# Kernel tuning notes

Measured on AMD Instinct MI355X. Metric: run time of the kernel, lower is better.

## Reference

```python
import jax, jax.numpy as jnp
from jax import lax
import numpy as np

# 6D tensors: (N, C, h1, w1, h2, w2); weights: (Cout, Cin, k,k,k,k)
DN = lax.ConvDimensionNumbers(lhs_spec=(0, 1, 2, 3, 4, 5),
                              rhs_spec=(0, 1, 2, 3, 4, 5),
                              out_spec=(0, 1, 2, 3, 4, 5))


def conv4d_relu(x, w, b):
    # true 4D convolution, stride 1, SAME padding, then bias + ReLU
    y = lax.conv_general_dilated(x, w, window_strides=(1, 1, 1, 1),
                                 padding='SAME', dimension_numbers=DN)
    return jax.nn.relu(y + b.reshape(1, -1, 1, 1, 1, 1))


def _perm(x):
    # swap the two (h, w) spatial pairs of the correlation tensor
    return jnp.transpose(x, (0, 1, 4, 5, 2, 3))


def _sym(x, w, b):
    # symmetric_mode branch: f(x) + perm(f(perm(x)))
    return conv4d_relu(x, w, b) + _perm(conv4d_relu(_perm(x), w, b))


def setup_inputs() -> dict:
    key = jax.random.key(0)
    ks = jax.random.split(key, 9)
    B, S = 4, 20
    sc = 0.05
    return {
        'x':    jax.random.normal(ks[0], (B, 1, S, S, S, S), dtype=jnp.float32),
        'w0':   jax.random.normal(ks[1], (16, 1, 5, 5, 5, 5), dtype=jnp.float32) * sc,
        'b0':   jax.random.normal(ks[2], (16,), dtype=jnp.float32) * sc,
        'w10':  jax.random.normal(ks[3], (8, 16, 3, 3, 5, 5), dtype=jnp.float32) * sc,
        'b10':  jax.random.normal(ks[4], (8,), dtype=jnp.float32) * sc,
        'w11':  jax.random.normal(ks[5], (8, 16, 5, 5, 5, 5), dtype=jnp.float32) * sc,
        'b11':  jax.random.normal(ks[6], (8,), dtype=jnp.float32) * sc,
        'w2':   jax.random.normal(ks[7], (1, 16, 5, 5, 5, 5), dtype=jnp.float32) * sc,
        'b2':   jax.random.normal(ks[8], (1,), dtype=jnp.float32) * sc,
    }


def reference(x, w0, b0, w10, b10, w11, b11, w2, b2):
    x = _sym(x, w0, b0)                       # [B,16,S,S,S,S]
    x0 = _sym(x, w10, b10)                    # [B, 8,S,S,S,S]
    x1 = _sym(x, w11, b11)                    # [B, 8,S,S,S,S]
    x = jnp.concatenate((x0, x1), axis=1)     # [B,16,S,S,S,S]
    return _sym(x, w2, b2)                    # [B, 1,S,S,S,S]
```

## Files before the change

### kernel.cpp

```cpp
#include <hip/hip_runtime.h>

#define TS 20
#define TS2 400

typedef __attribute__((ext_vector_type(8))) __bf16 bf16x8;
typedef __attribute__((ext_vector_type(4))) __bf16 bf16x4;
typedef __attribute__((ext_vector_type(4))) float  f32x4;
typedef __attribute__((ext_vector_type(4))) int    int4v;

__device__ __forceinline__ float relu_f(float v) { return v > 0.0f ? v : 0.0f; }

#define MFMA16(a, b, c) __builtin_amdgcn_mfma_f32_16x16x32_bf16((a), (b), (c), 0, 0, 0)

#define LPAD 580

__global__ __launch_bounds__(256)
void pack_w0(const float* __restrict__ w0, __bf16* __restrict__ wpk0)
{
    int idx = blockIdx.x * 256 + (int)threadIdx.x;
    if (idx >= 25 * 32 * 32) return;
    const int c = idx & 31;
    const int m = (idx >> 5) & 31;
    const int e = idx >> 10;
    float v = 0.0f;
    if (c < 25) {
        const int co = m & 15;
        const int k1o = c / 5, k2o = c % 5, k3i = e / 5, k4i = e % 5;
        if (m < 16) v = w0[co * 625 + k1o * 125 + k2o * 25 + k3i * 5 + k4i];
        else        v = w0[co * 625 + k3i * 125 + k4i * 25 + k1o * 5 + k2o];
    }
    wpk0[idx] = (__bf16)v;
}

__global__ __launch_bounds__(256)
void pack_wmid(const float* __restrict__ w10, const float* __restrict__ w11,
               __bf16* __restrict__ wpk)
{
    int idx = blockIdx.x * 256 + (int)threadIdx.x;
    if (idx >= 650 * 512) return;
    const int ci  = idx & 15;
    const int m   = (idx >> 4) & 31;
    const int off = idx >> 9;
    const int inner = off % 26, outer = off / 26;
    const int d1 = outer / 5 - 2, d2 = outer % 5 - 2;
    float v = 0.0f;
    if (inner < 25) {
        const int d3 = inner / 5 - 2, d4 = inner % 5 - 2;
        const int co = m & 7;
        const bool isB  = (m & 8)  != 0;
        const bool is11 = (m & 16) != 0;
        if (is11) {
            int k1, k2, k3, k4;
            if (!isB) { k1 = d1 + 2; k2 = d2 + 2; k3 = d3 + 2; k4 = d4 + 2; }
            else      { k1 = d3 + 2; k2 = d4 + 2; k3 = d1 + 2; k4 = d2 + 2; }
            v = w11[((((co * 16 + ci) * 5 + k1) * 5 + k2) * 5 + k3) * 5 + k4];
        } else {
            if (!isB) {
                if (d1 >= -1 && d1 <= 1 && d2 >= -1 && d2 <= 1)
                    v = w10[((((co * 16 + ci) * 3 + (d1 + 1)) * 3 + (d2 + 1)) * 5 + (d3 + 2)) * 5 + (d4 + 2)];
            } else {
                if (d3 >= -1 && d3 <= 1 && d4 >= -1 && d4 <= 1)
                    v = w10[((((co * 16 + ci) * 3 + (d3 + 1)) * 3 + (d4 + 1)) * 5 + (d1 + 2)) * 5 + (d2 + 2)];
            }
        }
    }
    wpk[idx] = (__bf16)v;
}

__global__ __launch_bounds__(256)
void pack_w2f(const float* __restrict__ w2, __bf16* __restrict__ wpk2f)
{
    int idx = blockIdx.x * 256 + (int)threadIdx.x;
    if (idx >= 26 * 64 * 16) return;
    const int ci = idx & 15;
    const int m  = (idx >> 4) & 63;
    const int e  = idx >> 10;
    float v = 0.0f;
    if (e < 25) {
        if (m < 25)
            v = w2[ci * 625 + (m / 5) * 125 + (m % 5) * 25 + (e / 5) * 5 + (e % 5)];
        else if (m >= 32 && m < 57) {
            const int dd = m - 32;
            v = w2[ci * 625 + (e / 5) * 125 + (e % 5) * 25 + (dd / 5) * 5 + (dd % 5)];
        }
    }
    wpk2f[idx] = (__bf16)v;
}

__global__ __launch_bounds__(320)
void conv0_mfma(const float* __restrict__ x, const __bf16* __restrict__ wpk0,
                const float* __restrict__ b0, __bf16* __restrict__ y1)
{
    __shared__ __bf16 lds0[4 * LPAD * 8];

    const int tid  = (int)threadIdx.x;
    const int lane = tid & 63;
    const int wave = tid >> 6;
    const int bid  = blockIdx.x;
    const int o2 = bid % TS, o1 = (bid / TS) % TS, n = bid / TS2;

    for (int i = tid; i < 4 * LPAD * 8 / 2; i += 320) ((int*)lds0)[i] = 0;
    __syncthreads();

    for (int c = tid; c < 25 * TS2; c += 320) {
        const int pl = c / TS2, pt = c % TS2;
        const int i1 = o1 + pl / 5 - 2, i2 = o2 + pl % 5 - 2;
        if (i1 >= 0 && i1 < TS && i2 >= 0 && i2 < TS) {
            const float v = x[(size_t)((n * TS + i1) * TS + i2) * TS2 + pt];
            const int L = (pt / TS + 2) * 24 + (pt % TS + 2);
            lds0[((pl >> 3) * LPAD + L) * 8 + (pl & 7)] = (__bf16)v;
        }
    }
    __syncthreads();

    const int mrow = lane & 15;
    const int sub  = lane >> 4;

    int sb[5];
#pragma unroll
    for (int i = 0; i < 5; ++i) {
        const int p = (wave * 5 + i) * 16 + mrow;
        sb[i] = (sub * LPAD + (p / TS + 2) * 24 + (p % TS + 2)) * 8;
    }

    f32x4 acc0[5], acc1[5];
#pragma unroll
    for (int i = 0; i < 5; ++i) {
        acc0[i] = (f32x4){0.f, 0.f, 0.f, 0.f};
        acc1[i] = (f32x4){0.f, 0.f, 0.f, 0.f};
    }

    bf16x8 a0 = *(const bf16x8*)(wpk0 + (size_t)mrow * 32 + sub * 8);
    bf16x8 a1 = *(const bf16x8*)(wpk0 + (size_t)(16 + mrow) * 32 + sub * 8);
    for (int e = 0; e < 25; ++e) {
        bf16x8 na0 = a0, na1 = a1;
        if (e < 24) {
            na0 = *(const bf16x8*)(wpk0 + ((size_t)((e + 1) * 32 + mrow)) * 32 + sub * 8);
            na1 = *(const bf16x8*)(wpk0 + ((size_t)((e + 1) * 32 + 16 + mrow)) * 32 + sub * 8);
        }
        const int delta = ((e / 5 - 2) * 24 + (e % 5 - 2)) * 8;
#pragma unroll
        for (int i = 0; i < 5; ++i) {
            bf16x8 bfr = *(const bf16x8*)(&lds0[sb[i] + delta]);
            acc0[i] = MFMA16(a0, bfr, acc0[i]);
            acc1[i] = MFMA16(a1, bfr, acc1[i]);
        }
        a0 = na0; a1 = na1;
    }

    const f32x4 bv = *(const f32x4*)(b0 + sub * 4);
#pragma unroll
    for (int i = 0; i < 5; ++i) {
        const int p = (wave * 5 + i) * 16 + mrow;
        bf16x4 pk;
#pragma unroll
        for (int r = 0; r < 4; ++r)
            pk[r] = (__bf16)(relu_f(acc0[i][r] + bv[r]) + relu_f(acc1[i][r] + bv[r]));
        *(bf16x4*)(y1 + ((size_t)bid * TS2 + p) * 16 + sub * 4) = pk;
    }
}

__global__ __launch_bounds__(320)
void conv4d_mid_mfma(const __bf16* __restrict__ y1, const __bf16* __restrict__ wpk,
                     const float* __restrict__ b10, const float* __restrict__ b11,
                     __bf16* __restrict__ y2)
{
    __shared__ __bf16 lds[4][9216];

    const int tid  = (int)threadIdx.x;
    const int lane = tid & 63;
    const int wave = tid >> 6;
    const int bid0 = blockIdx.x;
    const int bid  = (bid0 & 7) * 200 + (bid0 >> 3);
    const int o2 = bid % TS, o1 = (bid / TS) % TS, n = bid / TS2;

    for (int i = tid; i < 4 * 9216 / 2; i += 320) ((int*)lds)[i] = 0;

    const int mrow = lane & 15;
    const int sub  = lane >> 4;
    const int ci0  = (sub & 1) * 8;
    const int aoff = (sub >> 1) * 512 + mrow * 16 + ci0;

    int sbase[5];
#pragma unroll
    for (int i = 0; i < 5; ++i) {
        const int p  = (wave * 5 + i) * 16 + mrow;
        sbase[i] = ((p / TS + 2) * 24 + (p % TS + 2)) * 16 + ci0;
    }

    f32x4 acc[5][2];
#pragma unroll
    for (int i = 0; i < 5; ++i) {
        acc[i][0] = (f32x4){0.f, 0.f, 0.f, 0.f};
        acc[i][1] = (f32x4){0.f, 0.f, 0.f, 0.f};
    }

    const __bf16* ybase = y1 + (size_t)n * TS2 * TS2 * 16;

    auto nextv = [&](int k) {
        while (k < 25) {
            const int i1 = o1 + k / 5 - 2, i2 = o2 + k % 5 - 2;
            if (i1 >= 0 && i1 < TS && i2 >= 0 && i2 < TS) break;
            ++k;
        }
        return k;
    };
    auto stage = [&](int k, int bi) {
        const __bf16* src = ybase + (size_t)((o1 + k / 5 - 2) * TS + (o2 + k % 5 - 2)) * TS2 * 16;
        for (int c = tid; c < 800; c += 320) {
            const int h = c / 40, rem = c % 40;
            *(int4v*)(&lds[bi][((h + 2) * 24 + 2) * 16 + rem * 8]) =
                *(const int4v*)(src + c * 8);
        }
    };
    auto compute = [&](int k, int bi) {
        const __bf16* wbase = wpk + (size_t)k * 26 * 512;
        bf16x8 a0 = *(const bf16x8*)(wbase + aoff);
        bf16x8 a1 = *(const bf16x8*)(wbase + aoff + 256);
        for (int ic = 0; ic < 13; ++ic) {
            bf16x8 na0 = a0, na1 = a1;
            if (ic < 12) {
                na0 = *(const bf16x8*)(wbase + (ic + 1) * 1024 + aoff);
                na1 = *(const bf16x8*)(wbase + (ic + 1) * 1024 + aoff + 256);
            }
            const int e = 2 * ic + (sub >> 1);
            int d3 = 0, d4 = 0;
            if (e < 25) { d3 = e / 5 - 2; d4 = e % 5 - 2; }
            const int delta = (d3 * 24 + d4) * 16;
#pragma unroll
            for (int i = 0; i < 5; ++i) {
                bf16x8 bfr = *(const bf16x8*)(&lds[bi][sbase[i] + delta]);
                acc[i][0] = MFMA16(a0, bfr, acc[i][0]);
                acc[i][1] = MFMA16(a1, bfr, acc[i][1]);
            }
            a0 = na0; a1 = na1;
        }
    };

    __syncthreads();

    int kk = nextv(0);
    int pair = 0;
    while (kk < 25) {
        const int k2 = nextv(kk + 1);
        stage(kk, 2 * pair);
        if (k2 < 25) stage(k2, 2 * pair + 1);
        __syncthreads();
        compute(kk, 2 * pair);
        if (k2 < 25) compute(k2, 2 * pair + 1);
        pair ^= 1;
        kk = (k2 < 25) ? nextv(k2 + 1) : 25;
    }

    const size_t base = (size_t)bid * TS2 * 16;
#pragma unroll
    for (int i = 0; i < 5; ++i) {
        const int p = (wave * 5 + i) * 16 + mrow;
#pragma unroll
        for (int mt = 0; mt < 2; ++mt) {
            const float* bs = mt ? b11 : b10;
            const f32x4 bv = *(const f32x4*)(bs + (sub & 1) * 4);
            bf16x4 pk;
#pragma unroll
            for (int r = 0; r < 4; ++r) {
                float v = relu_f(acc[i][mt][r] + bv[r]);
                float o = v + __shfl_xor(v, 32);
                pk[r] = (__bf16)o;
            }
            if (lane < 32)
                *(bf16x4*)(y2 + base + (size_t)p * 16 + mt * 8 + (sub & 1) * 4) = pk;
        }
    }
}

__global__ __launch_bounds__(320)
void conv2t_mfma(const __bf16* __restrict__ y2, const __bf16* __restrict__ wpk2f,
                 int n0, __bf16* __restrict__ t)
{
    __shared__ __bf16 lds[2 * LPAD * 8];

    const int tid  = (int)threadIdx.x;
    const int lane = tid & 63;
    const int wave = tid >> 6;
    const int bid = blockIdx.x;
    const int q2 = bid % TS, q1 = (bid / TS) % TS, nl = bid / TS2;

    for (int i = tid; i < 2 * LPAD * 8 / 2; i += 320) ((int*)lds)[i] = 0;
    __syncthreads();

    const __bf16* src = y2 + (size_t)(((n0 + nl) * TS + q1) * TS + q2) * TS2 * 16;
    for (int c = tid; c < 800; c += 320) {
        const int h = c / 40, rem = c % 40;
        const int w = rem >> 1, cb = rem & 1;
        int4v v = *(const int4v*)(src + c * 8);
        *(int4v*)(&lds[(cb * LPAD + (h + 2) * 24 + 2 + w) * 8]) = v;
    }
    __syncthreads();

    const int mrow = lane & 15;
    const int sub  = lane >> 4;

    int sbase[5];
#pragma unroll
    for (int i = 0; i < 5; ++i) {
        const int p  = (wave * 5 + i) * 16 + mrow;
        sbase[i] = ((sub & 1) * LPAD + (p / TS + 2) * 24 + (p % TS + 2)) * 8;
    }

    f32x4 acc[5][4];
#pragma unroll
    for (int i = 0; i < 5; ++i)
#pragma unroll
        for (int mt = 0; mt < 4; ++mt)
            acc[i][mt] = (f32x4){0.f, 0.f, 0.f, 0.f};

    for (int ic = 0; ic < 13; ++ic) {
        const int e = 2 * ic + (sub >> 1);
        int d3 = 0, d4 = 0;
        if (e < 25) { d3 = e / 5 - 2; d4 = e % 5 - 2; }
        const int delta = (d3 * 24 + d4) * 8;
        const __bf16* abase = wpk2f + ((size_t)e * 64 + mrow) * 16 + (sub & 1) * 8;
        bf16x8 a0 = *(const bf16x8*)(abase);
        bf16x8 a1 = *(const bf16x8*)(abase + 256);
        bf16x8 a2 = *(const bf16x8*)(abase + 512);
        bf16x8 a3 = *(const bf16x8*)(abase + 768);
#pragma unroll
        for (int i = 0; i < 5; ++i) {
            bf16x8 bfr = *(const bf16x8*)(&lds[sbase[i] + delta]);
            acc[i][0] = MFMA16(a0, bfr, acc[i][0]);
            acc[i][1] = MFMA16(a1, bfr, acc[i][1]);
            acc[i][2] = MFMA16(a2, bfr, acc[i][2]);
            acc[i][3] = MFMA16(a3, bfr, acc[i][3]);
        }
    }

    __bf16* tb = t + (size_t)((nl * TS + q1) * TS + q2) * (50 * TS2);
#pragma unroll
    for (int i = 0; i < 5; ++i) {
        const int p = (wave * 5 + i) * 16 + mrow;
#pragma unroll
        for (int mt = 0; mt < 4; ++mt) {
#pragma unroll
            for (int r = 0; r < 4; ++r) {
                const int gm = mt * 16 + sub * 4 + r;
                int m50 = -1;
                if (gm < 25) m50 = gm;
                else if (gm >= 32 && gm < 57) m50 = gm - 7;
                if (m50 >= 0) tb[m50 * TS2 + p] = (__bf16)acc[i][mt][r];
            }
        }
    }
}

__global__ __launch_bounds__(448)
void conv2_sum(const __bf16* __restrict__ t, const float* __restrict__ b2,
               int n0, float* __restrict__ out)
{
    const int tid = (int)threadIdx.x;
    if (tid >= TS2) return;
    const int bid = blockIdx.x;
    const int o2 = bid % TS, o1 = (bid / TS) % TS, nl = bid / TS2;

    float accA = 0.0f, accB = 0.0f;
    for (int dd = 0; dd < 25; ++dd) {
        const int q1 = o1 + dd / 5 - 2, q2 = o2 + dd % 5 - 2;
        if (q1 < 0 || q1 >= TS || q2 < 0 || q2 >= TS) continue;
        const __bf16* tb = t + (size_t)((nl * TS + q1) * TS + q2) * (50 * TS2) + tid;
        accA += (float)tb[dd * TS2];
        accB += (float)tb[(25 + dd) * TS2];
    }
    const float bias = b2[0];
    out[(size_t)(n0 + nl) * (TS2 * (size_t)TS2) + (size_t)(o1 * TS + o2) * TS2 + tid] =
        relu_f(accA + bias) + relu_f(accB + bias);
}

extern "C" void kernel_launch(void* const* d_in, const int* in_sizes, int n_in,
                              void* d_out, int out_size, void* d_ws, size_t ws_size,
                              hipStream_t stream)
{
    const float* x   = (const float*)d_in[0];
    const float* w0  = (const float*)d_in[1];
    const float* b0  = (const float*)d_in[2];
    const float* w10 = (const float*)d_in[3];
    const float* b10 = (const float*)d_in[4];
    const float* w11 = (const float*)d_in[5];
    const float* b11 = (const float*)d_in[6];
    const float* w2  = (const float*)d_in[7];
    const float* b2  = (const float*)d_in[8];
    float* out = (float*)d_out;

    __bf16* y1    = (__bf16*)d_ws;
    __bf16* y2    = y1 + (size_t)10240000;
    __bf16* tbuf  = y2 + (size_t)10240000;
    __bf16* wpkm  = tbuf + (size_t)16000000;
    __bf16* wpk0  = wpkm + 650 * 512;
    __bf16* wpk2f = wpk0 + 25 * 32 * 32;

    dim3 blk320(320), blk256(256), blk448(448);

    pack_w0  <<<dim3((25600 + 255) / 256),  blk256, 0, stream>>>(w0, wpk0);
    pack_wmid<<<dim3((332800 + 255) / 256), blk256, 0, stream>>>(w10, w11, wpkm);
    pack_w2f <<<dim3((26624 + 255) / 256),  blk256, 0, stream>>>(w2, wpk2f);

    conv0_mfma     <<<dim3(4 * TS * TS), blk320, 0, stream>>>(x, wpk0, b0, y1);
    conv4d_mid_mfma<<<dim3(1600),        blk320, 0, stream>>>(y1, wpkm, b10, b11, y2);

    for (int n0 = 0; n0 < 4; n0 += 2) {
        conv2t_mfma<<<dim3(800), blk320, 0, stream>>>(y2, wpk2f, n0, tbuf);
        conv2_sum  <<<dim3(800), blk448, 0, stream>>>(tbuf, b2, n0, out);
    }
}
```

Measured before the change: 604.3 us.

## Store y1 zero-padded and stream per-wave slices to LDS with async loads

conv0 now writes y1 into zero-padded 24x24 planes, cleared beforehand by a new zero kernel, so the mid conv needs no halo handling or LDS clearing. Each wave of the mid conv fetches only the rows its pixels need into its own double-buffered LDS region, using global_load_lds direct-to-LDS transfers. This removes the block-wide __syncthreads and the register staging, and lets each wave prefetch the next input plane while computing the current one. The cost is an extra zero-fill pass over a larger padded buffer, overlapping halo rows loaded by several waves, and a dependence on correct wait handling for the async LDS loads.

Measured after the change: 658.7 us. +9.0%, slower.

```diff
diff --git a/kernel.cpp b/kernel.cpp
--- a/kernel.cpp
+++ b/kernel.cpp
@@ -2,6 +2,7 @@
 
 #define TS 20
 #define TS2 400
+#define PLANE 9216
 
 typedef __attribute__((ext_vector_type(8))) __bf16 bf16x8;
 typedef __attribute__((ext_vector_type(4))) __bf16 bf16x4;
@@ -11,6 +12,13 @@
 __device__ __forceinline__ float relu_f(float v) { return v > 0.0f ? v : 0.0f; }
 
 #define MFMA16(a, b, c) __builtin_amdgcn_mfma_f32_16x16x32_bf16((a), (b), (c), 0, 0, 0)
+
+__device__ __forceinline__ void gload_lds16(const __bf16* g, __bf16* l)
+{
+    __builtin_amdgcn_global_load_lds(
+        (const __attribute__((address_space(1))) void*)g,
+        (__attribute__((address_space(3))) void*)l, 16, 0, 0);
+}
 
 #define LPAD 580
 
@@ -87,6 +95,14 @@
     wpk2f[idx] = (__bf16)v;
 }
 
+__global__ __launch_bounds__(256)
+void zero_y1p(int4v* __restrict__ dst, int n16)
+{
+    const int stride = gridDim.x * 256;
+    for (int i = blockIdx.x * 256 + (int)threadIdx.x; i < n16; i += stride)
+        dst[i] = (int4v){0, 0, 0, 0};
+}
+
 __global__ __launch_bounds__(320)
 void conv0_mfma(const float* __restrict__ x, const __bf16* __restrict__ wpk0,
                 const float* __restrict__ b0, __bf16* __restrict__ y1)
@@ -152,11 +168,12 @@
 #pragma unroll
     for (int i = 0; i < 5; ++i) {
         const int p = (wave * 5 + i) * 16 + mrow;
+        const int Lp = (p / TS + 2) * 24 + (p % TS + 2);
         bf16x4 pk;
 #pragma unroll
         for (int r = 0; r < 4; ++r)
             pk[r] = (__bf16)(relu_f(acc0[i][r] + bv[r]) + relu_f(acc1[i][r] + bv[r]));
-        *(bf16x4*)(y1 + ((size_t)bid * TS2 + p) * 16 + sub * 4) = pk;
+        *(bf16x4*)(y1 + (size_t)bid * PLANE + Lp * 16 + sub * 4) = pk;
     }
 }
 
@@ -165,7 +182,7 @@
                      const float* __restrict__ b10, const float* __restrict__ b11,
                      __bf16* __restrict__ y2)
 {
-    __shared__ __bf16 lds[4][9216];
+    __shared__ __bf16 lds[5][2][3072];
 
     const int tid  = (int)threadIdx.x;
     const int lane = tid & 63;
@@ -174,8 +191,6 @@
     const int bid  = (bid0 & 7) * 200 + (bid0 >> 3);
     const int o2 = bid % TS, o1 = (bid / TS) % TS, n = bid / TS2;
 
-    for (int i = tid; i < 4 * 9216 / 2; i += 320) ((int*)lds)[i] = 0;
-
     const int mrow = lane & 15;
     const int sub  = lane >> 4;
     const int ci0  = (sub & 1) * 8;
@@ -184,8 +199,8 @@
     int sbase[5];
 #pragma unroll
     for (int i = 0; i < 5; ++i) {
-        const int p  = (wave * 5 + i) * 16 + mrow;
-        sbase[i] = ((p / TS + 2) * 24 + (p % TS + 2)) * 16 + ci0;
+        const int pl = i * 16 + mrow;
+        sbase[i] = ((pl / TS + 2) * 24 + (pl % TS + 2)) * 16 + ci0;
     }
 
     f32x4 acc[5][2];
@@ -195,7 +210,8 @@
         acc[i][1] = (f32x4){0.f, 0.f, 0.f, 0.f};
     }
 
-    const __bf16* ybase = y1 + (size_t)n * TS2 * TS2 * 16;
+    const __bf16* ybase = y1 + (size_t)n * TS2 * PLANE;
+    const int sliceoff = wave * 1536 + lane * 8;
 
     auto nextv = [&](int k) {
         while (k < 25) {
@@ -205,15 +221,14 @@
         }
         return k;
     };
-    auto stage = [&](int k, int bi) {
-        const __bf16* src = ybase + (size_t)((o1 + k / 5 - 2) * TS + (o2 + k % 5 - 2)) * TS2 * 16;
-        for (int c = tid; c < 800; c += 320) {
-            const int h = c / 40, rem = c % 40;
-            *(int4v*)(&lds[bi][((h + 2) * 24 + 2) * 16 + rem * 8]) =
-                *(const int4v*)(src + c * 8);
-        }
+    auto dma = [&](int k, int b) {
+        const __bf16* src = ybase
+            + (size_t)((o1 + k / 5 - 2) * TS + (o2 + k % 5 - 2)) * PLANE + sliceoff;
+#pragma unroll
+        for (int i = 0; i < 6; ++i)
+            gload_lds16(src + i * 512, &lds[wave][b][i * 512]);
     };
-    auto compute = [&](int k, int bi) {
+    auto compute = [&](int k, int b) {
         const __bf16* wbase = wpk + (size_t)k * 26 * 512;
         bf16x8 a0 = *(const bf16x8*)(wbase + aoff);
         bf16x8 a1 = *(const bf16x8*)(wbase + aoff + 256);
@@ -229,7 +244,7 @@
             const int delta = (d3 * 24 + d4) * 16;
 #pragma unroll
             for (int i = 0; i < 5; ++i) {
-                bf16x8 bfr = *(const bf16x8*)(&lds[bi][sbase[i] + delta]);
+                bf16x8 bfr = *(const bf16x8*)(&lds[wave][b][sbase[i] + delta]);
                 acc[i][0] = MFMA16(a0, bfr, acc[i][0]);
                 acc[i][1] = MFMA16(a1, bfr, acc[i][1]);
             }
@@ -237,19 +252,17 @@
         }
     };
 
-    __syncthreads();
-
     int kk = nextv(0);
-    int pair = 0;
+    if (kk < 25) dma(kk, 0);
     while (kk < 25) {
-        const int k2 = nextv(kk + 1);
-        stage(kk, 2 * pair);
-        if (k2 < 25) stage(k2, 2 * pair + 1);
-        __syncthreads();
-        compute(kk, 2 * pair);
-        if (k2 < 25) compute(k2, 2 * pair + 1);
-        pair ^= 1;
-        kk = (k2 < 25) ? nextv(k2 + 1) : 25;
+        const int k1 = nextv(kk + 1);
+        if (k1 < 25) dma(k1, 1);
+        compute(kk, 0);
+        if (k1 >= 25) break;
+        const int k2 = nextv(k1 + 1);
+        if (k2 < 25) dma(k2, 0);
+        compute(k1, 1);
+        kk = k2;
     }
 
     const size_t base = (size_t)bid * TS2 * 16;
@@ -389,10 +402,10 @@
     const float* b2  = (const float*)d_in[8];
     float* out = (float*)d_out;
 
-    __bf16* y1    = (__bf16*)d_ws;
-    __bf16* y2    = y1 + (size_t)10240000;
-    __bf16* tbuf  = y2 + (size_t)10240000;
-    __bf16* wpkm  = tbuf + (size_t)16000000;
+    __bf16* y1p   = (__bf16*)d_ws;
+    __bf16* tbuf  = (__bf16*)d_ws;
+    __bf16* y2    = (__bf16*)d_ws + 16000000;
+    __bf16* wpkm  = y2 + 10240000;
     __bf16* wpk0  = wpkm + 650 * 512;
     __bf16* wpk2f = wpk0 + 25 * 32 * 32;
 
@@ -402,8 +415,11 @@
     pack_wmid<<<dim3((332800 + 255) / 256), blk256, 0, stream>>>(w10, w11, wpkm);
     pack_w2f <<<dim3((26624 + 255) / 256),  blk256, 0, stream>>>(w2, wpk2f);
 
-    conv0_mfma     <<<dim3(4 * TS * TS), blk320, 0, stream>>>(x, wpk0, b0, y1);
-    conv4d_mid_mfma<<<dim3(1600),        blk320, 0, stream>>>(y1, wpkm, b10, b11, y2);
+    zero_y1p<<<dim3(2048), blk256, 0, stream>>>((int4v*)y1p,
+        (int)((size_t)4 * TS2 * PLANE * 2 / 16));
+
+    conv0_mfma     <<<dim3(4 * TS * TS), blk320, 0, stream>>>(x, wpk0, b0, y1p);
+    conv4d_mid_mfma<<<dim3(1600),        blk320, 0, stream>>>(y1p, wpkm, b10, b11, y2);
 
     for (int n0 = 0; n0 < 4; n0 += 2) {
         conv2t_mfma<<<dim3(800), blk320, 0, stream>>>(y2, wpk2f, n0, tbuf);
```
